# Performance work log

Hardware: AMD Instinct MI355X
Metric: run time of the kernel (lower is better)

Reference implementation:

```python
import jax, jax.numpy as jnp
import numpy as np

N, H, E = 50000, 128, 1600000

def setup_inputs() -> dict:
    key = jax.random.key(0)
    k1, k2, k3, k4 = jax.random.split(key, 4)
    h = jax.random.normal(k1, (N, H), dtype=jnp.float32)
    edge_index = jax.random.randint(k2, (2, E), 0, N, dtype=jnp.int64)
    # edge_scorer: Linear(2H, 1); node_scorer: Linear(H, 1)
    W_edge = jax.random.normal(k3, (2 * H, 1), dtype=jnp.float32) / np.sqrt(2 * H)
    b_edge = jnp.zeros((1,), dtype=jnp.float32)
    W_node = jax.random.normal(k4, (H, 1), dtype=jnp.float32) / np.sqrt(H)
    b_node = jnp.zeros((1,), dtype=jnp.float32)
    return {"h": h, "edge_index": edge_index, "W_edge": W_edge,
            "b_edge": b_edge, "W_node": W_node, "b_node": b_node}

def reference(h, edge_index, W_edge, b_edge, W_node, b_node):
    n = h.shape[0]
    src, dst = edge_index[0], edge_index[1]
    # cat([h[src], h[dst]]) @ W_edge == (h @ W_src)[src] + (h @ W_dst)[dst]
    # (same math as the torch module, avoids materializing the (E, 2H) concat)
    W_src, W_dst = W_edge[:h.shape[1]], W_edge[h.shape[1]:]
    s_src = (h @ W_src)[:, 0]            # (N,)
    s_dst = (h @ W_dst)[:, 0]            # (N,)
    edge_scores = s_src[src] + s_dst[dst] + b_edge[0]   # (E,)
    node_edge_score = jax.ops.segment_sum(edge_scores, dst, num_segments=n)
    node_self_score = (h @ W_node)[:, 0] + b_node[0]    # (N,)
    combined = node_edge_score + node_self_score
    return jax.nn.softmax(combined, axis=0)
```

## Files before the change

kernel.cpp:

```cpp
#include <hip/hip_runtime.h>
#include <math.h>


#define RANGE_BITS 14
#define RANGE_SIZE (1 << RANGE_BITS)
#define NCHUNKS 64
#define STAT_BLOCKS 256

typedef float vfloat4 __attribute__((ext_vector_type(4)));
typedef unsigned vuint4 __attribute__((ext_vector_type(4)));

__global__ __launch_bounds__(256) void node_scores_kernel(
    const float* __restrict__ h,
    const float* __restrict__ W_edge,
    const float* __restrict__ b_edge,
    const float* __restrict__ W_node,
    const float* __restrict__ b_node,
    float* __restrict__ s_src,
    float* __restrict__ t_dst,
    float* __restrict__ self_sc,
    float* __restrict__ acc,
    int N, int H)
{
    const int lane16 = threadIdx.x & 15;
    const int n = (blockIdx.x * blockDim.x + threadIdx.x) >> 4;
    if (n >= N) return;

    const float4* __restrict__ h4  = (const float4*)(h + (size_t)n * H);
    const float4* __restrict__ ws4 = (const float4*)(W_edge);
    const float4* __restrict__ wd4 = (const float4*)(W_edge + H);
    const float4* __restrict__ wn4 = (const float4*)(W_node);
    const int H4 = H >> 2;

    float ps = 0.0f, pd = 0.0f, pn = 0.0f;
    for (int i = lane16; i < H4; i += 16) {
        float4 hv = h4[i];
        float4 a = ws4[i], b = wd4[i], c = wn4[i];
        ps = fmaf(hv.x, a.x, fmaf(hv.y, a.y, fmaf(hv.z, a.z, fmaf(hv.w, a.w, ps))));
        pd = fmaf(hv.x, b.x, fmaf(hv.y, b.y, fmaf(hv.z, b.z, fmaf(hv.w, b.w, pd))));
        pn = fmaf(hv.x, c.x, fmaf(hv.y, c.y, fmaf(hv.z, c.z, fmaf(hv.w, c.w, pn))));
    }
    #pragma unroll
    for (int off = 8; off > 0; off >>= 1) {
        ps += __shfl_xor(ps, off, 64);
        pd += __shfl_xor(pd, off, 64);
        pn += __shfl_xor(pn, off, 64);
    }
    if (lane16 == 0) {
        float self = pn + b_node[0];
        s_src[n]   = ps;
        t_dst[n]   = pd + b_edge[0];
        self_sc[n] = self;
        acc[n]     = self;
    }
}

__global__ __launch_bounds__(1024) void edge_bin_cnt_kernel(
    const int* __restrict__ ei,
    const float* __restrict__ s_src,
    const float* __restrict__ t_dst,
    float* __restrict__ partials,
    int N, int E, int chunk, int vec_ok)
{
    extern __shared__ char smem_raw[];
    float*    __restrict__ hsum = (float*)smem_raw;
    unsigned* __restrict__ hcnt = (unsigned*)(smem_raw + (RANGE_SIZE << 2));

    const int id = blockIdx.x;
    const int g  = id & 7;
    const int s  = id >> 3;
    const int b  = (g << 3) | (s & 7);
    const int r  = s >> 3;
    const int lo = r << RANGE_BITS;
    const int hi = min(lo + RANGE_SIZE, N);
    const unsigned span = (unsigned)(hi - lo);

    {
        vfloat4* __restrict__ hz = (vfloat4*)hsum;
        vuint4*  __restrict__ cz = (vuint4*)hcnt;
        const vfloat4 zf = {0.0f, 0.0f, 0.0f, 0.0f};
        const vuint4  zu = {0u, 0u, 0u, 0u};
        for (int i = threadIdx.x; i < (RANGE_SIZE >> 2); i += blockDim.x) {
            hz[i] = zf;
            cz[i] = zu;
        }
    }
    __syncthreads();

    const int e0 = b * chunk;
    const int e1 = min(e0 + chunk, E);
    if (e0 < e1) {
        if (vec_ok) {
            const int nvec = (e1 - e0) >> 2;
            const int4* __restrict__ dst4 = (const int4*)(ei + E + e0);
            const int4* __restrict__ src4 = (const int4*)(ei + e0);
            int i = threadIdx.x;
            for (; i + (int)blockDim.x < nvec; i += 2 * blockDim.x) {
                int4 da = dst4[i];
                int4 db = dst4[i + blockDim.x];
                int4 sa = src4[i];
                int4 sb = src4[i + blockDim.x];
                unsigned ax = (unsigned)(da.x - lo), ay = (unsigned)(da.y - lo);
                unsigned az = (unsigned)(da.z - lo), aw = (unsigned)(da.w - lo);
                if (ax < span) { atomicAdd(&hsum[ax], s_src[sa.x]); atomicAdd(&hcnt[ax], 1u); }
                if (ay < span) { atomicAdd(&hsum[ay], s_src[sa.y]); atomicAdd(&hcnt[ay], 1u); }
                if (az < span) { atomicAdd(&hsum[az], s_src[sa.z]); atomicAdd(&hcnt[az], 1u); }
                if (aw < span) { atomicAdd(&hsum[aw], s_src[sa.w]); atomicAdd(&hcnt[aw], 1u); }
                unsigned bx = (unsigned)(db.x - lo), by = (unsigned)(db.y - lo);
                unsigned bz = (unsigned)(db.z - lo), bw = (unsigned)(db.w - lo);
                if (bx < span) { atomicAdd(&hsum[bx], s_src[sb.x]); atomicAdd(&hcnt[bx], 1u); }
                if (by < span) { atomicAdd(&hsum[by], s_src[sb.y]); atomicAdd(&hcnt[by], 1u); }
                if (bz < span) { atomicAdd(&hsum[bz], s_src[sb.z]); atomicAdd(&hcnt[bz], 1u); }
                if (bw < span) { atomicAdd(&hsum[bw], s_src[sb.w]); atomicAdd(&hcnt[bw], 1u); }
            }
            if (i < nvec) {
                int4 da = dst4[i];
                int4 sa = src4[i];
                unsigned ax = (unsigned)(da.x - lo), ay = (unsigned)(da.y - lo);
                unsigned az = (unsigned)(da.z - lo), aw = (unsigned)(da.w - lo);
                if (ax < span) { atomicAdd(&hsum[ax], s_src[sa.x]); atomicAdd(&hcnt[ax], 1u); }
                if (ay < span) { atomicAdd(&hsum[ay], s_src[sa.y]); atomicAdd(&hcnt[ay], 1u); }
                if (az < span) { atomicAdd(&hsum[az], s_src[sa.z]); atomicAdd(&hcnt[az], 1u); }
                if (aw < span) { atomicAdd(&hsum[aw], s_src[sa.w]); atomicAdd(&hcnt[aw], 1u); }
            }
            for (int e = e0 + 4 * nvec + threadIdx.x; e < e1; e += blockDim.x) {
                int d = ei[E + e];
                unsigned u = (unsigned)(d - lo);
                if (u < span) { atomicAdd(&hsum[u], s_src[ei[e]]); atomicAdd(&hcnt[u], 1u); }
            }
        } else {
            for (int e = e0 + threadIdx.x; e < e1; e += blockDim.x) {
                int d = ei[E + e];
                unsigned u = (unsigned)(d - lo);
                if (u < span) { atomicAdd(&hsum[u], s_src[ei[e]]); atomicAdd(&hcnt[u], 1u); }
            }
        }
    }
    __syncthreads();

    float* __restrict__ outp = partials + (size_t)b * N + lo;
    const float* __restrict__ td = t_dst + lo;
    const int len = hi - lo;
    for (int i = threadIdx.x; i < len; i += blockDim.x) {
        unsigned c = hcnt[i];
        outp[i] = fmaf(__uint2float_rn(c), td[i], hsum[i]);
    }
}

__global__ __launch_bounds__(1024) void edge_bin_swz_kernel(
    const int* __restrict__ ei,
    const float* __restrict__ s_src,
    const float* __restrict__ t_dst,
    float* __restrict__ partials,
    int N, int E, int chunk, int vec_ok)
{
    __shared__ float hist[RANGE_SIZE];
    const int id = blockIdx.x;
    const int g  = id & 7;
    const int s  = id >> 3;
    const int b  = (g << 3) | (s & 7);
    const int r  = s >> 3;
    const int lo = r << RANGE_BITS;
    const int hi = min(lo + RANGE_SIZE, N);
    const unsigned span = (unsigned)(hi - lo);

    {
        vfloat4* __restrict__ hz = (vfloat4*)hist;
        const vfloat4 z = {0.0f, 0.0f, 0.0f, 0.0f};
        for (int i = threadIdx.x; i < (RANGE_SIZE >> 2); i += blockDim.x)
            hz[i] = z;
    }
    __syncthreads();

    const int e0 = b * chunk;
    const int e1 = min(e0 + chunk, E);
    if (e0 < e1) {
        if (vec_ok) {
            const int nvec = (e1 - e0) >> 2;
            const int4* __restrict__ dst4 = (const int4*)(ei + E + e0);
            const int4* __restrict__ src4 = (const int4*)(ei + e0);
            int i = threadIdx.x;
            for (; i + (int)blockDim.x < nvec; i += 2 * blockDim.x) {
                int4 da = dst4[i];
                int4 db = dst4[i + blockDim.x];
                int4 sa = src4[i];
                int4 sb = src4[i + blockDim.x];
                unsigned ax = (unsigned)(da.x - lo), ay = (unsigned)(da.y - lo);
                unsigned az = (unsigned)(da.z - lo), aw = (unsigned)(da.w - lo);
                if (ax < span) atomicAdd(&hist[ax], s_src[sa.x] + t_dst[da.x]);
                if (ay < span) atomicAdd(&hist[ay], s_src[sa.y] + t_dst[da.y]);
                if (az < span) atomicAdd(&hist[az], s_src[sa.z] + t_dst[da.z]);
                if (aw < span) atomicAdd(&hist[aw], s_src[sa.w] + t_dst[da.w]);
                unsigned bx = (unsigned)(db.x - lo), by = (unsigned)(db.y - lo);
                unsigned bz = (unsigned)(db.z - lo), bw = (unsigned)(db.w - lo);
                if (bx < span) atomicAdd(&hist[bx], s_src[sb.x] + t_dst[db.x]);
                if (by < span) atomicAdd(&hist[by], s_src[sb.y] + t_dst[db.y]);
                if (bz < span) atomicAdd(&hist[bz], s_src[sb.z] + t_dst[db.z]);
                if (bw < span) atomicAdd(&hist[bw], s_src[sb.w] + t_dst[db.w]);
            }
            if (i < nvec) {
                int4 da = dst4[i];
                int4 sa = src4[i];
                unsigned ax = (unsigned)(da.x - lo), ay = (unsigned)(da.y - lo);
                unsigned az = (unsigned)(da.z - lo), aw = (unsigned)(da.w - lo);
                if (ax < span) atomicAdd(&hist[ax], s_src[sa.x] + t_dst[da.x]);
                if (ay < span) atomicAdd(&hist[ay], s_src[sa.y] + t_dst[da.y]);
                if (az < span) atomicAdd(&hist[az], s_src[sa.z] + t_dst[da.z]);
                if (aw < span) atomicAdd(&hist[aw], s_src[sa.w] + t_dst[da.w]);
            }
            for (int e = e0 + 4 * nvec + threadIdx.x; e < e1; e += blockDim.x) {
                int d = ei[E + e];
                unsigned u = (unsigned)(d - lo);
                if (u < span) atomicAdd(&hist[u], s_src[ei[e]] + t_dst[d]);
            }
        } else {
            for (int e = e0 + threadIdx.x; e < e1; e += blockDim.x) {
                int d = ei[E + e];
                unsigned u = (unsigned)(d - lo);
                if (u < span) atomicAdd(&hist[u], s_src[ei[e]] + t_dst[d]);
            }
        }
    }
    __syncthreads();

    float* __restrict__ outp = partials + (size_t)b * N + lo;
    const int len = hi - lo;
    if ((len & 3) == 0) {
        const int len4 = len >> 2;
        const vfloat4* __restrict__ h4 = (const vfloat4*)hist;
        vfloat4* __restrict__ o4 = (vfloat4*)outp;
        for (int i = threadIdx.x; i < len4; i += blockDim.x) o4[i] = h4[i];
    } else {
        for (int i = threadIdx.x; i < len; i += blockDim.x) outp[i] = hist[i];
    }
}

__global__ __launch_bounds__(1024) void edge_bin_kernel(
    const int* __restrict__ ei,
    const float* __restrict__ s_src,
    const float* __restrict__ t_dst,
    float* __restrict__ partials,
    int N, int E, int chunk, int vec_ok)
{
    __shared__ float hist[RANGE_SIZE];
    const int b  = blockIdx.x;
    const int r  = blockIdx.y;
    const int lo = r << RANGE_BITS;
    const int hi = min(lo + RANGE_SIZE, N);
    const unsigned span = (unsigned)(hi - lo);

    for (int i = threadIdx.x; i < RANGE_SIZE; i += blockDim.x) hist[i] = 0.0f;
    __syncthreads();

    const int e0 = b * chunk;
    const int e1 = min(e0 + chunk, E);
    for (int e = e0 + threadIdx.x; e < e1; e += blockDim.x) {
        int d = ei[E + e];
        unsigned u = (unsigned)(d - lo);
        if (u < span) atomicAdd(&hist[u], s_src[ei[e]] + t_dst[d]);
    }
    __syncthreads();

    float* __restrict__ outp = partials + (size_t)b * N + lo;
    const int len = hi - lo;
    for (int i = threadIdx.x; i < len; i += blockDim.x) outp[i] = hist[i];
}

__global__ __launch_bounds__(256) void edge_accum_fallback_kernel(
    const int* __restrict__ ei,
    const float* __restrict__ s_src,
    const float* __restrict__ t_dst,
    float* __restrict__ acc,
    int E)
{
    int e = blockIdx.x * blockDim.x + threadIdx.x;
    if (e >= E) return;
    int s = ei[e];
    int d = ei[E + e];
    atomicAdd(&acc[d], s_src[s] + t_dst[d]);
}

__device__ __forceinline__ float blockReduceMaxB(float v) {
    __shared__ float sm[16];
    #pragma unroll
    for (int off = 32; off > 0; off >>= 1) v = fmaxf(v, __shfl_xor(v, off, 64));
    const int w = threadIdx.x >> 6, l = threadIdx.x & 63;
    const int nw = blockDim.x >> 6;
    if (l == 0) sm[w] = v;
    __syncthreads();
    float r = sm[0];
    for (int i = 1; i < nw; ++i) r = fmaxf(r, sm[i]);
    __syncthreads();
    return r;
}

__device__ __forceinline__ float blockReduceSumB(float v) {
    __shared__ float sm[16];
    #pragma unroll
    for (int off = 32; off > 0; off >>= 1) v += __shfl_xor(v, off, 64);
    const int w = threadIdx.x >> 6, l = threadIdx.x & 63;
    const int nw = blockDim.x >> 6;
    if (l == 0) sm[w] = v;
    __syncthreads();
    float r = 0.0f;
    for (int i = 0; i < nw; ++i) r += sm[i];
    __syncthreads();
    return r;
}

__global__ __launch_bounds__(256) void combine_stats_kernel(
    const float* __restrict__ self_sc,
    const float* __restrict__ partials,
    float* __restrict__ acc,
    float* __restrict__ red,
    int N, int B, int use_partials)
{
    float m = -INFINITY, l = 0.0f;
    for (int i = blockIdx.x * blockDim.x + threadIdx.x; i < N;
         i += gridDim.x * blockDim.x) {
        float v;
        if (use_partials) {
            float v0 = self_sc[i], v1 = 0.0f, v2 = 0.0f, v3 = 0.0f;
            int b = 0;
            for (; b + 4 <= B; b += 4) {
                v0 += partials[(size_t)(b + 0) * N + i];
                v1 += partials[(size_t)(b + 1) * N + i];
                v2 += partials[(size_t)(b + 2) * N + i];
                v3 += partials[(size_t)(b + 3) * N + i];
            }
            for (; b < B; ++b) v0 += partials[(size_t)b * N + i];
            v = (v0 + v1) + (v2 + v3);
            acc[i] = v;
        } else {
            v = acc[i];
        }
        float nm = fmaxf(m, v);
        l = l * __expf(m - nm) + __expf(v - nm);
        m = nm;
    }
    float mb = blockReduceMaxB(m);
    float ladj = (m == -INFINITY) ? 0.0f : l * __expf(m - mb);
    float lb = blockReduceSumB(ladj);
    if (threadIdx.x == 0) {
        red[blockIdx.x] = mb;
        red[STAT_BLOCKS + blockIdx.x] = lb;
    }
}

__global__ __launch_bounds__(256) void finalize_kernel(
    const float* __restrict__ acc,
    const float* __restrict__ red,
    float* __restrict__ out,
    int N)
{
    float m = red[threadIdx.x];
    float l = red[STAT_BLOCKS + threadIdx.x];
    float M = blockReduceMaxB(m);
    float L = blockReduceSumB(l * __expf(m - M));
    const float inv = 1.0f / L;

    int i = blockIdx.x * blockDim.x + threadIdx.x;
    if (i < N) out[i] = __expf(acc[i] - M) * inv;
}

extern "C" void kernel_launch(void* const* d_in, const int* in_sizes, int n_in,
                              void* d_out, int out_size, void* d_ws, size_t ws_size,
                              hipStream_t stream) {
    const float* h      = (const float*)d_in[0];
    const int*   ei     = (const int*)  d_in[1];
    const float* W_edge = (const float*)d_in[2];
    const float* b_edge = (const float*)d_in[3];
    const float* W_node = (const float*)d_in[4];
    const float* b_node = (const float*)d_in[5];

    const int H = in_sizes[2] / 2;
    const int N = in_sizes[0] / H;
    const int E = in_sizes[1] / 2;

    float* out      = (float*)d_out;
    float* ws       = (float*)d_ws;
    float* s_src    = ws;
    float* t_dst    = ws + (size_t)N;
    float* self_s   = ws + 2 * (size_t)N;
    float* acc      = ws + 3 * (size_t)N;
    float* red      = ws + 4 * (size_t)N;
    float* partials = red + 2 * STAT_BLOCKS;

    const size_t base_floats = 4 * (size_t)N + 2 * STAT_BLOCKS;
    int B = 0;
    if (ws_size / sizeof(float) > base_floats) {
        size_t avail = ws_size / sizeof(float) - base_floats;
        B = (int)(avail / (size_t)N);
    }
    if (B > NCHUNKS) B = NCHUNKS;
    const int R = (N + RANGE_SIZE - 1) >> RANGE_BITS;
    const int use_partials = (B >= 16) ? 1 : 0;

    const int want_lds = (RANGE_SIZE << 2) * 2;
    int dev = 0;
    hipGetDevice(&dev);
    int optin = 0, maxsh = 0;
    hipDeviceGetAttribute(&optin, hipDeviceAttributeSharedMemPerBlockOptin, dev);
    hipDeviceGetAttribute(&maxsh, hipDeviceAttributeMaxSharedMemoryPerBlock, dev);
    int use_cnt = (optin >= want_lds || maxsh >= want_lds) ? 1 : 0;
    if (use_cnt) {
        use_cnt = (hipFuncSetAttribute((const void*)edge_bin_cnt_kernel,
                                       hipFuncAttributeMaxDynamicSharedMemorySize,
                                       want_lds) == hipSuccess) ? 1 : 0;
    }

    {
        int threads = N * 16;
        int grid = (threads + 255) / 256;
        node_scores_kernel<<<grid, 256, 0, stream>>>(
            h, W_edge, b_edge, W_node, b_node,
            s_src, t_dst, self_s, acc, N, H);
    }
    if (use_partials) {
        int chunk = (((E + B - 1) / B) + 3) & ~3;
        int vec_ok = ((E & 3) == 0) ? 1 : 0;
        if (B == NCHUNKS && R == 4) {
            if (use_cnt) {
                edge_bin_cnt_kernel<<<256, 1024, want_lds, stream>>>(
                    ei, s_src, t_dst, partials, N, E, chunk, vec_ok);
            } else {
                edge_bin_swz_kernel<<<256, 1024, 0, stream>>>(
                    ei, s_src, t_dst, partials, N, E, chunk, vec_ok);
            }
        } else {
            dim3 grid(B, R);
            edge_bin_kernel<<<grid, 1024, 0, stream>>>(
                ei, s_src, t_dst, partials, N, E, chunk, vec_ok);
        }
    } else {
        int grid = (E + 255) / 256;
        edge_accum_fallback_kernel<<<grid, 256, 0, stream>>>(ei, s_src, t_dst, acc, E);
    }
    combine_stats_kernel<<<STAT_BLOCKS, 256, 0, stream>>>(
        self_s, partials, acc, red, N, B, use_partials);
    {
        int grid = (N + 255) / 256;
        finalize_kernel<<<grid, 256, 0, stream>>>(acc, red, out, N);
    }
}
```

Before: 115.4 us.

## Use two 32K-node LDS histogram ranges with 128 edge chunks

```diff
diff --git a/kernel.cpp b/kernel.cpp
--- a/kernel.cpp
+++ b/kernel.cpp
@@ -4,11 +4,12 @@
 
 #define RANGE_BITS 14
 #define RANGE_SIZE (1 << RANGE_BITS)
-#define NCHUNKS 64
+#define RANGE_BITS2 15
+#define RANGE_SIZE2 (1 << RANGE_BITS2)
+#define NCHUNKS 128
 #define STAT_BLOCKS 256
 
 typedef float vfloat4 __attribute__((ext_vector_type(4)));
-typedef unsigned vuint4 __attribute__((ext_vector_type(4)));
 
 __global__ __launch_bounds__(256) void node_scores_kernel(
     const float* __restrict__ h,
@@ -55,119 +56,28 @@
     }
 }
 
-__global__ __launch_bounds__(1024) void edge_bin_cnt_kernel(
+__global__ __launch_bounds__(1024) void edge_bin_r2_kernel(
     const int* __restrict__ ei,
     const float* __restrict__ s_src,
     const float* __restrict__ t_dst,
     float* __restrict__ partials,
     int N, int E, int chunk, int vec_ok)
 {
-    extern __shared__ char smem_raw[];
-    float*    __restrict__ hsum = (float*)smem_raw;
-    unsigned* __restrict__ hcnt = (unsigned*)(smem_raw + (RANGE_SIZE << 2));
+    extern __shared__ float hist[];
 
     const int id = blockIdx.x;
     const int g  = id & 7;
     const int s  = id >> 3;
-    const int b  = (g << 3) | (s & 7);
-    const int r  = s >> 3;
-    const int lo = r << RANGE_BITS;
-    const int hi = min(lo + RANGE_SIZE, N);
-    const unsigned span = (unsigned)(hi - lo);
-
-    {
-        vfloat4* __restrict__ hz = (vfloat4*)hsum;
-        vuint4*  __restrict__ cz = (vuint4*)hcnt;
-        const vfloat4 zf = {0.0f, 0.0f, 0.0f, 0.0f};
-        const vuint4  zu = {0u, 0u, 0u, 0u};
-        for (int i = threadIdx.x; i < (RANGE_SIZE >> 2); i += blockDim.x) {
-            hz[i] = zf;
-            cz[i] = zu;
-        }
-    }
-    __syncthreads();
-
-    const int e0 = b * chunk;
-    const int e1 = min(e0 + chunk, E);
-    if (e0 < e1) {
-        if (vec_ok) {
-            const int nvec = (e1 - e0) >> 2;
-            const int4* __restrict__ dst4 = (const int4*)(ei + E + e0);
-            const int4* __restrict__ src4 = (const int4*)(ei + e0);
-            int i = threadIdx.x;
-            for (; i + (int)blockDim.x < nvec; i += 2 * blockDim.x) {
-                int4 da = dst4[i];
-                int4 db = dst4[i + blockDim.x];
-                int4 sa = src4[i];
-                int4 sb = src4[i + blockDim.x];
-                unsigned ax = (unsigned)(da.x - lo), ay = (unsigned)(da.y - lo);
-                unsigned az = (unsigned)(da.z - lo), aw = (unsigned)(da.w - lo);
-                if (ax < span) { atomicAdd(&hsum[ax], s_src[sa.x]); atomicAdd(&hcnt[ax], 1u); }
-                if (ay < span) { atomicAdd(&hsum[ay], s_src[sa.y]); atomicAdd(&hcnt[ay], 1u); }
-                if (az < span) { atomicAdd(&hsum[az], s_src[sa.z]); atomicAdd(&hcnt[az], 1u); }
-                if (aw < span) { atomicAdd(&hsum[aw], s_src[sa.w]); atomicAdd(&hcnt[aw], 1u); }
-                unsigned bx = (unsigned)(db.x - lo), by = (unsigned)(db.y - lo);
-                unsigned bz = (unsigned)(db.z - lo), bw = (unsigned)(db.w - lo);
-                if (bx < span) { atomicAdd(&hsum[bx], s_src[sb.x]); atomicAdd(&hcnt[bx], 1u); }
-                if (by < span) { atomicAdd(&hsum[by], s_src[sb.y]); atomicAdd(&hcnt[by], 1u); }
-                if (bz < span) { atomicAdd(&hsum[bz], s_src[sb.z]); atomicAdd(&hcnt[bz], 1u); }
-                if (bw < span) { atomicAdd(&hsum[bw], s_src[sb.w]); atomicAdd(&hcnt[bw], 1u); }
-            }
-            if (i < nvec) {
-                int4 da = dst4[i];
-                int4 sa = src4[i];
-                unsigned ax = (unsigned)(da.x - lo), ay = (unsigned)(da.y - lo);
-                unsigned az = (unsigned)(da.z - lo), aw = (unsigned)(da.w - lo);
-                if (ax < span) { atomicAdd(&hsum[ax], s_src[sa.x]); atomicAdd(&hcnt[ax], 1u); }
-                if (ay < span) { atomicAdd(&hsum[ay], s_src[sa.y]); atomicAdd(&hcnt[ay], 1u); }
-                if (az < span) { atomicAdd(&hsum[az], s_src[sa.z]); atomicAdd(&hcnt[az], 1u); }
-                if (aw < span) { atomicAdd(&hsum[aw], s_src[sa.w]); atomicAdd(&hcnt[aw], 1u); }
-            }
-            for (int e = e0 + 4 * nvec + threadIdx.x; e < e1; e += blockDim.x) {
-                int d = ei[E + e];
-                unsigned u = (unsigned)(d - lo);
-                if (u < span) { atomicAdd(&hsum[u], s_src[ei[e]]); atomicAdd(&hcnt[u], 1u); }
-            }
-        } else {
-            for (int e = e0 + threadIdx.x; e < e1; e += blockDim.x) {
-                int d = ei[E + e];
-                unsigned u = (unsigned)(d - lo);
-                if (u < span) { atomicAdd(&hsum[u], s_src[ei[e]]); atomicAdd(&hcnt[u], 1u); }
-            }
-        }
-    }
-    __syncthreads();
-
-    float* __restrict__ outp = partials + (size_t)b * N + lo;
-    const float* __restrict__ td = t_dst + lo;
-    const int len = hi - lo;
-    for (int i = threadIdx.x; i < len; i += blockDim.x) {
-        unsigned c = hcnt[i];
-        outp[i] = fmaf(__uint2float_rn(c), td[i], hsum[i]);
-    }
-}
-
-__global__ __launch_bounds__(1024) void edge_bin_swz_kernel(
-    const int* __restrict__ ei,
-    const float* __restrict__ s_src,
-    const float* __restrict__ t_dst,
-    float* __restrict__ partials,
-    int N, int E, int chunk, int vec_ok)
-{
-    __shared__ float hist[RANGE_SIZE];
-    const int id = blockIdx.x;
-    const int g  = id & 7;
-    const int s  = id >> 3;
-    const int b  = (g << 3) | (s & 7);
-    const int r  = s >> 3;
-    const int lo = r << RANGE_BITS;
-    const int hi = min(lo + RANGE_SIZE, N);
+    const int b  = (g << 4) | (s & 15);
+    const int r  = s >> 4;
+    const int lo = r << RANGE_BITS2;
+    const int hi = min(lo + RANGE_SIZE2, N);
     const unsigned span = (unsigned)(hi - lo);
 
     {
         vfloat4* __restrict__ hz = (vfloat4*)hist;
         const vfloat4 z = {0.0f, 0.0f, 0.0f, 0.0f};
-        for (int i = threadIdx.x; i < (RANGE_SIZE >> 2); i += blockDim.x)
+        for (int i = threadIdx.x; i < (RANGE_SIZE2 >> 2); i += blockDim.x)
             hz[i] = z;
     }
     __syncthreads();
@@ -235,6 +145,94 @@
     }
 }
 
+__global__ __launch_bounds__(1024) void edge_bin_swz_kernel(
+    const int* __restrict__ ei,
+    const float* __restrict__ s_src,
+    const float* __restrict__ t_dst,
+    float* __restrict__ partials,
+    int N, int E, int chunk, int vec_ok)
+{
+    __shared__ float hist[RANGE_SIZE];
+    const int id = blockIdx.x;
+    const int g  = id & 7;
+    const int s  = id >> 3;
+    const int b  = (g << 3) | (s & 7);
+    const int r  = s >> 3;
+    const int lo = r << RANGE_BITS;
+    const int hi = min(lo + RANGE_SIZE, N);
+    const unsigned span = (unsigned)(hi - lo);
+
+    {
+        vfloat4* __restrict__ hz = (vfloat4*)hist;
+        const vfloat4 z = {0.0f, 0.0f, 0.0f, 0.0f};
+        for (int i = threadIdx.x; i < (RANGE_SIZE >> 2); i += blockDim.x)
+            hz[i] = z;
+    }
+    __syncthreads();
+
+    const int e0 = b * chunk;
+    const int e1 = min(e0 + chunk, E);
+    if (e0 < e1) {
+        if (vec_ok) {
+            const int nvec = (e1 - e0) >> 2;
+            const int4* __restrict__ dst4 = (const int4*)(ei + E + e0);
+            const int4* __restrict__ src4 = (const int4*)(ei + e0);
+            int i = threadIdx.x;
+            for (; i + (int)blockDim.x < nvec; i += 2 * blockDim.x) {
+                int4 da = dst4[i];
+                int4 db = dst4[i + blockDim.x];
+                int4 sa = src4[i];
+                int4 sb = src4[i + blockDim.x];
+                unsigned ax = (unsigned)(da.x - lo), ay = (unsigned)(da.y - lo);
+                unsigned az = (unsigned)(da.z - lo), aw = (unsigned)(da.w - lo);
+                if (ax < span) atomicAdd(&hist[ax], s_src[sa.x] + t_dst[da.x]);
+                if (ay < span) atomicAdd(&hist[ay], s_src[sa.y] + t_dst[da.y]);
+                if (az < span) atomicAdd(&hist[az], s_src[sa.z] + t_dst[da.z]);
+                if (aw < span) atomicAdd(&hist[aw], s_src[sa.w] + t_dst[da.w]);
+                unsigned bx = (unsigned)(db.x - lo), by = (unsigned)(db.y - lo);
+                unsigned bz = (unsigned)(db.z - lo), bw = (unsigned)(db.w - lo);
+                if (bx < span) atomicAdd(&hist[bx], s_src[sb.x] + t_dst[db.x]);
+                if (by < span) atomicAdd(&hist[by], s_src[sb.y] + t_dst[db.y]);
+                if (bz < span) atomicAdd(&hist[bz], s_src[sb.z] + t_dst[db.z]);
+                if (bw < span) atomicAdd(&hist[bw], s_src[sb.w] + t_dst[db.w]);
+            }
+            if (i < nvec) {
+                int4 da = dst4[i];
+                int4 sa = src4[i];
+                unsigned ax = (unsigned)(da.x - lo), ay = (unsigned)(da.y - lo);
+                unsigned az = (unsigned)(da.z - lo), aw = (unsigned)(da.w - lo);
+                if (ax < span) atomicAdd(&hist[ax], s_src[sa.x] + t_dst[da.x]);
+                if (ay < span) atomicAdd(&hist[ay], s_src[sa.y] + t_dst[da.y]);
+                if (az < span) atomicAdd(&hist[az], s_src[sa.z] + t_dst[da.z]);
+                if (aw < span) atomicAdd(&hist[aw], s_src[sa.w] + t_dst[da.w]);
+            }
+            for (int e = e0 + 4 * nvec + threadIdx.x; e < e1; e += blockDim.x) {
+                int d = ei[E + e];
+                unsigned u = (unsigned)(d - lo);
+                if (u < span) atomicAdd(&hist[u], s_src[ei[e]] + t_dst[d]);
+            }
+        } else {
+            for (int e = e0 + threadIdx.x; e < e1; e += blockDim.x) {
+                int d = ei[E + e];
+                unsigned u = (unsigned)(d - lo);
+                if (u < span) atomicAdd(&hist[u], s_src[ei[e]] + t_dst[d]);
+            }
+        }
+    }
+    __syncthreads();
+
+    float* __restrict__ outp = partials + (size_t)b * N + lo;
+    const int len = hi - lo;
+    if ((len & 3) == 0) {
+        const int len4 = len >> 2;
+        const vfloat4* __restrict__ h4 = (const vfloat4*)hist;
+        vfloat4* __restrict__ o4 = (vfloat4*)outp;
+        for (int i = threadIdx.x; i < len4; i += blockDim.x) o4[i] = h4[i];
+    } else {
+        for (int i = threadIdx.x; i < len; i += blockDim.x) outp[i] = hist[i];
+    }
+}
+
 __global__ __launch_bounds__(1024) void edge_bin_kernel(
     const int* __restrict__ ei,
     const float* __restrict__ s_src,
@@ -387,27 +385,32 @@
     float* partials = red + 2 * STAT_BLOCKS;
 
     const size_t base_floats = 4 * (size_t)N + 2 * STAT_BLOCKS;
-    int B = 0;
+    int Bcap = 0;
     if (ws_size / sizeof(float) > base_floats) {
         size_t avail = ws_size / sizeof(float) - base_floats;
-        B = (int)(avail / (size_t)N);
-    }
-    if (B > NCHUNKS) B = NCHUNKS;
-    const int R = (N + RANGE_SIZE - 1) >> RANGE_BITS;
-    const int use_partials = (B >= 16) ? 1 : 0;
-
-    const int want_lds = (RANGE_SIZE << 2) * 2;
+        Bcap = (int)(avail / (size_t)N);
+    }
+
+    const int want_lds = RANGE_SIZE2 * 4;
     int dev = 0;
     hipGetDevice(&dev);
     int optin = 0, maxsh = 0;
     hipDeviceGetAttribute(&optin, hipDeviceAttributeSharedMemPerBlockOptin, dev);
     hipDeviceGetAttribute(&maxsh, hipDeviceAttributeMaxSharedMemoryPerBlock, dev);
-    int use_cnt = (optin >= want_lds || maxsh >= want_lds) ? 1 : 0;
-    if (use_cnt) {
-        use_cnt = (hipFuncSetAttribute((const void*)edge_bin_cnt_kernel,
-                                       hipFuncAttributeMaxDynamicSharedMemorySize,
-                                       want_lds) == hipSuccess) ? 1 : 0;
-    }
+    int lds_ok = (optin >= want_lds || maxsh >= want_lds) ? 1 : 0;
+    if (lds_ok) {
+        lds_ok = (hipFuncSetAttribute((const void*)edge_bin_r2_kernel,
+                                      hipFuncAttributeMaxDynamicSharedMemorySize,
+                                      want_lds) == hipSuccess) ? 1 : 0;
+    }
+    const int use_r2 = (lds_ok && Bcap >= NCHUNKS && N <= 2 * RANGE_SIZE2) ? 1 : 0;
+
+    int B;
+    if (use_r2)            B = NCHUNKS;
+    else if (Bcap >= 64)   B = 64;
+    else                   B = (Bcap > 0) ? Bcap : 0;
+    const int R4 = (N + RANGE_SIZE - 1) >> RANGE_BITS;
+    const int use_partials = (B >= 16) ? 1 : 0;
 
     {
         int threads = N * 16;
@@ -419,16 +422,14 @@
     if (use_partials) {
         int chunk = (((E + B - 1) / B) + 3) & ~3;
         int vec_ok = ((E & 3) == 0) ? 1 : 0;
-        if (B == NCHUNKS && R == 4) {
-            if (use_cnt) {
-                edge_bin_cnt_kernel<<<256, 1024, want_lds, stream>>>(
-                    ei, s_src, t_dst, partials, N, E, chunk, vec_ok);
-            } else {
-                edge_bin_swz_kernel<<<256, 1024, 0, stream>>>(
-                    ei, s_src, t_dst, partials, N, E, chunk, vec_ok);
-            }
+        if (use_r2) {
+            edge_bin_r2_kernel<<<256, 1024, want_lds, stream>>>(
+                ei, s_src, t_dst, partials, N, E, chunk, vec_ok);
+        } else if (B == 64 && R4 == 4) {
+            edge_bin_swz_kernel<<<256, 1024, 0, stream>>>(
+                ei, s_src, t_dst, partials, N, E, chunk, vec_ok);
         } else {
-            dim3 grid(B, R);
+            dim3 grid(B, R4);
             edge_bin_kernel<<<grid, 1024, 0, stream>>>(
                 ei, s_src, t_dst, partials, N, E, chunk, vec_ok);
         }
```

Result: slower. 121.2 us (+5.0%).
